# Optimization experiments

Measured on AMD Instinct MI355X. Metric: run time of the kernel, lower is better.

Reference implementation:

```python
import jax, jax.numpy as jnp
import numpy as np

N_NODES = 100000
N_EDGES = 1600000
N_GRAPHS = 256
F_IN = 128
NEURON = 64
AF = 8  # attention_num_feature


def gcn_conv(h_in, W, b, src, dst, n):
    # PyG GCNConv: add self loops, symmetric normalization, XW then aggregate, + bias
    h = h_in @ W  # [N, out]
    loop = jnp.arange(n)
    s = jnp.concatenate([src, loop])
    d = jnp.concatenate([dst, loop])
    deg = jax.ops.segment_sum(jnp.ones(s.shape[0], h.dtype), d, num_segments=n)
    dis = jax.lax.rsqrt(deg)  # deg >= 1 because of self loops
    norm = dis[s] * dis[d]  # [E+N]
    msg = h[s] * norm[:, None]
    out = jax.ops.segment_sum(msg, d, num_segments=n)
    return out + b


def setup_inputs() -> dict:
    key = jax.random.key(0)
    ks = jax.random.split(key, 16)
    x = jax.random.normal(ks[0], (N_NODES, F_IN), dtype=jnp.float32)
    closeness = jax.random.normal(ks[1], (N_NODES, AF), dtype=jnp.float32)
    edge_index = jax.random.randint(ks[2], (2, N_EDGES), 0, N_NODES, dtype=jnp.int64)
    batch = jnp.sort(jax.random.randint(ks[3], (N_NODES,), 0, N_GRAPHS, dtype=jnp.int64))
    def lin(k, fi, fo):
        lim = 1.0 / np.sqrt(fi)
        return jax.random.uniform(k, (fi, fo), jnp.float32, -lim, lim)
    return {
        "x": x, "closeness": closeness,
        "W1": lin(ks[4], F_IN, NEURON), "b1": jnp.zeros((NEURON,), jnp.float32),
        "W2": lin(ks[5], NEURON, NEURON), "b2": jnp.zeros((NEURON,), jnp.float32),
        "W3": lin(ks[6], NEURON, NEURON), "b3": jnp.zeros((NEURON,), jnp.float32),
        "Wc": lin(ks[7], AF, 1), "bc": jnp.zeros((1,), jnp.float32),
        "Wa1": lin(ks[8], NEURON, 16), "ba1": jnp.zeros((16,), jnp.float32),
        "Wa2": lin(ks[9], 16, 1), "ba2": jnp.zeros((1,), jnp.float32),
        "edge_index": edge_index, "batch": batch,
    }


def reference(x, closeness, W1, b1, W2, b2, W3, b3, Wc, bc, Wa1, ba1, Wa2, ba2, edge_index, batch):
    n, G = x.shape[0], N_GRAPHS
    src, dst = edge_index[0], edge_index[1]
    h = jax.nn.relu(gcn_conv(x, W1, b1, src, dst, n))
    h = jax.nn.relu(gcn_conv(h, W2, b2, src, dst, n))
    h = jax.nn.relu(gcn_conv(h, W3, b3, src, dst, n))  # [N, 64]
    # per-graph softmax over closeness logits (vectorized form of the python loop)
    logits = (closeness @ Wc + bc)[:, 0]  # [N]
    m = jax.ops.segment_max(logits, batch, num_segments=G)
    e = jnp.exp(logits - m[batch])
    z = jax.ops.segment_sum(e, batch, num_segments=G)
    p = e / z[batch]  # softmax within each graph
    counts = jax.ops.segment_sum(jnp.ones((n,), h.dtype), batch, num_segments=G)
    counts = jnp.maximum(counts, 1.0)
    attn = p * counts[batch]  # softmax * curr_size
    # self_average: mean over nodes of attn * h  == segment_sum / count
    g = jax.ops.segment_sum(attn[:, None] * h, batch, num_segments=G) / counts[:, None]  # [G, 64]
    a = jax.nn.relu(g @ Wa1 + ba1)
    return a @ Wa2 + ba2  # [G, 1]
```

## Files before the change

kernel.cpp:

```cpp
#include <hip/hip_runtime.h>
#include <hip/hip_fp16.h>
#include <math.h>


#define BKT_SHIFT 7
#define BKT_NODES 128
#define BKT_CAP 4096
#define EPB 8192

typedef _Float16 f16x8 __attribute__((ext_vector_type(8)));
typedef float f32x4 __attribute__((ext_vector_type(4)));

__global__ __launch_bounds__(1024) void block_hist_kernel(
    const int* __restrict__ dst, int* __restrict__ hist, int E, int NBKT, int NBLK) {
  __shared__ int lh[1024];
  const int t = threadIdx.x;
  const int blk = blockIdx.x;
  for (int k = t; k < NBKT; k += 1024) lh[k] = 0;
  __syncthreads();
  const int e0 = blk * EPB;
  const int e1 = min(e0 + EPB, E);
  for (int e = e0 + t; e < e1; e += 1024) atomicAdd(&lh[dst[e] >> BKT_SHIFT], 1);
  __syncthreads();
  for (int k = t; k < NBKT; k += 1024) hist[k * NBLK + blk] = lh[k];
}

__global__ __launch_bounds__(256) void row_scan_kernel(
    const int* __restrict__ hist, int* __restrict__ ebase, int* __restrict__ btot,
    int NBLK) {
  __shared__ int sh[256];
  const int k = blockIdx.x;
  const int t = threadIdx.x;
  int v = (t < NBLK) ? hist[(long)k * NBLK + t] : 0;
  sh[t] = v;
  __syncthreads();
  for (int s = 1; s < 256; s <<= 1) {
    int add = (t >= s) ? sh[t - s] : 0;
    __syncthreads();
    sh[t] += add;
    __syncthreads();
  }
  if (t < NBLK) ebase[(long)k * NBLK + t] = sh[t] - v;
  if (t == 255) btot[k] = sh[255];
}

__global__ __launch_bounds__(1024) void bucket_scan_kernel(
    const int* __restrict__ btot, int* __restrict__ bbase, int E, int NBKT) {
  __shared__ int sh[1024];
  const int t = threadIdx.x;
  int v = (t < NBKT) ? btot[t] : 0;
  sh[t] = v;
  __syncthreads();
  for (int s = 1; s < 1024; s <<= 1) {
    int add = (t >= s) ? sh[t - s] : 0;
    __syncthreads();
    sh[t] += add;
    __syncthreads();
  }
  if (t < NBKT) bbase[t] = sh[t] - v;
  if (t == 0) bbase[NBKT] = E;
}

__global__ __launch_bounds__(1024) void group_kernel(
    const int* __restrict__ src, const int* __restrict__ dst,
    const int* __restrict__ bbase, const int* __restrict__ ebase,
    unsigned int* __restrict__ grouped, int E, int NBKT, int NBLK) {
  __shared__ int lcur[1024];
  const int t = threadIdx.x;
  const int blk = blockIdx.x;
  for (int k = t; k < NBKT; k += 1024)
    lcur[k] = bbase[k] + ebase[(long)k * NBLK + blk];
  __syncthreads();
  const int e0 = blk * EPB;
  const int e1 = min(e0 + EPB, E);
  for (int e = e0 + t; e < e1; e += 1024) {
    int d = dst[e];
    int b = d >> BKT_SHIFT;
    int pos = atomicAdd(&lcur[b], 1);
    grouped[pos] = ((unsigned int)(d & (BKT_NODES - 1)) << 17) | (unsigned int)src[e];
  }
}

__global__ __launch_bounds__(256) void bucket_build_kernel(
    const unsigned int* __restrict__ grouped, const int* __restrict__ bbase,
    int* __restrict__ csr_src, int* __restrict__ ends, float* __restrict__ dis, int N) {
  __shared__ int lcnt[BKT_NODES];
  __shared__ int lsum[BKT_NODES];
  __shared__ int lcur[BKT_NODES];
  __shared__ int stage[BKT_CAP];
  const int b = blockIdx.x;
  const int t = threadIdx.x;
  const int node0 = b << BKT_SHIFT;
  const int nn = min(BKT_NODES, N - node0);
  const int base = bbase[b];
  const int m = bbase[b + 1] - base;

  if (t < BKT_NODES) lcnt[t] = 0;
  __syncthreads();
  for (int i = t; i < m; i += 256) atomicAdd(&lcnt[grouped[base + i] >> 17], 1);
  __syncthreads();
  if (t < BKT_NODES) lsum[t] = lcnt[t];
  __syncthreads();
  for (int s = 1; s < BKT_NODES; s <<= 1) {
    int add = 0;
    if (t < BKT_NODES && t >= s) add = lsum[t - s];
    __syncthreads();
    if (t < BKT_NODES) lsum[t] += add;
    __syncthreads();
  }
  if (t < nn) {
    ends[node0 + t] = base + lsum[t];
    dis[node0 + t] = 1.0f / sqrtf((float)(lcnt[t] + 1));
    lcur[t] = lsum[t] - lcnt[t];
  }
  __syncthreads();
  if (m <= BKT_CAP) {
    for (int i = t; i < m; i += 256) {
      unsigned int v = grouped[base + i];
      int p = atomicAdd(&lcur[v >> 17], 1);
      stage[p] = (int)(v & 0x1FFFFu);
    }
    __syncthreads();
    for (int i = t; i < m; i += 256) csr_src[base + i] = stage[i];
  } else {
    for (int i = t; i < m; i += 256) {
      unsigned int v = grouped[base + i];
      int p = atomicAdd(&lcur[v >> 17], 1);
      csr_src[base + p] = (int)(v & 0x1FFFFu);
    }
  }
}


template <int K, typename Tin>
__global__ __launch_bounds__(256) void gemm_mfma_kernel(
    const Tin* __restrict__ H, const float* __restrict__ W,
    const float* __restrict__ dis, __half* __restrict__ C, int N) {
  __shared__ __align__(16) __half Hs[64 * K];
  __shared__ __align__(16) __half Ws[64 * K];
  const int t = threadIdx.x;
  const int rowBase = blockIdx.x * 64;

  if constexpr (sizeof(Tin) == 4) {
    const int NF4 = 64 * K / 4;
#pragma unroll
    for (int i = 0; i < NF4 / 256; ++i) {
      int f = t + i * 256;
      int row = f / (K / 4);
      int c4 = f % (K / 4);
      int gr = rowBase + row;
      float4 v = make_float4(0.f, 0.f, 0.f, 0.f);
      if (gr < N) v = *reinterpret_cast<const float4*>(H + (long)gr * K + c4 * 4);
      union { uint2 u; __half2 h[2]; } pk;
      pk.h[0] = __floats2half2_rn(v.x, v.y);
      pk.h[1] = __floats2half2_rn(v.z, v.w);
      int byte = (row * K + c4 * 4) * 2;
      byte ^= (row & 7) << 4;
      *reinterpret_cast<uint2*>(reinterpret_cast<char*>(Hs) + byte) = pk.u;
    }
  } else {
    const int NC = 64 * K / 8;
#pragma unroll
    for (int i = 0; i < NC / 256; ++i) {
      int f = t + i * 256;
      int row = f / (K / 8);
      int c8 = f % (K / 8);
      int gr = rowBase + row;
      uint4 v = make_uint4(0u, 0u, 0u, 0u);
      if (gr < N) v = *reinterpret_cast<const uint4*>(H + (long)gr * K + c8 * 8);
      int byte = (row * K + c8 * 8) * 2;
      byte ^= (row & 7) << 4;
      *reinterpret_cast<uint4*>(reinterpret_cast<char*>(Hs) + byte) = v;
    }
  }

  {
    const int NU = (K / 2) * 16;
#pragma unroll
    for (int i = 0; i < NU / 256; ++i) {
      int u = t + i * 256;
      int kp = u >> 4;
      int cq = u & 15;
      const float4 w0 = *reinterpret_cast<const float4*>(W + (long)(2 * kp) * 64 + cq * 4);
      const float4 w1 = *reinterpret_cast<const float4*>(W + (long)(2 * kp + 1) * 64 + cq * 4);
#pragma unroll
      for (int j = 0; j < 4; ++j) {
        int c = cq * 4 + j;
        __half2 p = __floats2half2_rn((&w0.x)[j], (&w1.x)[j]);
        int byte = (c * K + 2 * kp) * 2;
        byte ^= (c & 7) << 4;
        *reinterpret_cast<__half2*>(reinterpret_cast<char*>(Ws) + byte) = p;
      }
    }
  }
  __syncthreads();

  const int w = t >> 6;
  const int l = t & 63;
  const int r = l & 15;
  const int g = l >> 4;
  const int rowL = 16 * w + r;
  f32x4 acc[4] = {{0.f, 0.f, 0.f, 0.f}, {0.f, 0.f, 0.f, 0.f},
                  {0.f, 0.f, 0.f, 0.f}, {0.f, 0.f, 0.f, 0.f}};
#pragma unroll
  for (int s = 0; s < K / 32; ++s) {
    int abyte = (rowL * K + s * 32 + g * 8) * 2;
    abyte ^= (rowL & 7) << 4;
    f16x8 afrag = *reinterpret_cast<const f16x8*>(reinterpret_cast<const char*>(Hs) + abyte);
#pragma unroll
    for (int n = 0; n < 4; ++n) {
      int col = n * 16 + r;
      int bbyte = (col * K + s * 32 + g * 8) * 2;
      bbyte ^= (col & 7) << 4;
      f16x8 bfrag = *reinterpret_cast<const f16x8*>(reinterpret_cast<const char*>(Ws) + bbyte);
      acc[n] = __builtin_amdgcn_mfma_f32_16x16x32_f16(afrag, bfrag, acc[n], 0, 0, 0);
    }
  }

  const int outRow0 = rowBase + 16 * w + 4 * g;
#pragma unroll
  for (int j = 0; j < 4; ++j) {
    int row = outRow0 + j;
    if (row < N) {
      float dv = dis[row];
#pragma unroll
      for (int n = 0; n < 4; ++n) {
        C[(long)row * 64 + n * 16 + r] = __float2half(acc[n][j] * dv);
      }
    }
  }
}


__device__ __forceinline__ float4 h4_to_f4(uint2 u) {
  const __half2 lo = *reinterpret_cast<const __half2*>(&u.x);
  const __half2 hi = *reinterpret_cast<const __half2*>(&u.y);
  const float2 flo = __half22float2(lo);
  const float2 fhi = __half22float2(hi);
  return make_float4(flo.x, flo.y, fhi.x, fhi.y);
}

__global__ __launch_bounds__(256) void aggregate_kernel(
    const __half* __restrict__ Ts, const int* __restrict__ csr_src,
    const int* __restrict__ ends, const float* __restrict__ dis,
    const float* __restrict__ bias, __half* __restrict__ O, int N) {
  int gid = blockIdx.x * 256 + threadIdx.x;
  int d = gid >> 6;
  if (d >= N) return;
  const int lane = threadIdx.x & 63;
  const int q = lane >> 4;
  const int c = lane & 15;
  const int beg = (d == 0) ? 0 : ends[d - 1];
  const int m = ends[d] - beg;
  const uint2* Tv = (const uint2*)Ts;
  const int* sl = csr_src + beg;

  float4 a0 = make_float4(0.f, 0.f, 0.f, 0.f);
  float4 a1 = a0, a2 = a0, a3 = a0;
  if (q == 0) a0 = h4_to_f4(Tv[(long)d * 16 + c]);

  for (int base = 0; base < m; base += 64) {
    const int take = min(m - base, 64);
    int idx = (lane < take) ? sl[base + lane] : 0;
    for (int j = 0; j < take; j += 16) {
      const int l0 = j + q, l1 = j + 4 + q, l2 = j + 8 + q, l3 = j + 12 + q;
      int s0 = __shfl(idx, l0 & 63, 64);
      int s1 = __shfl(idx, l1 & 63, 64);
      int s2 = __shfl(idx, l2 & 63, 64);
      int s3 = __shfl(idx, l3 & 63, 64);
      uint2 r0 = Tv[(long)s0 * 16 + c];
      uint2 r1 = Tv[(long)s1 * 16 + c];
      uint2 r2 = Tv[(long)s2 * 16 + c];
      uint2 r3 = Tv[(long)s3 * 16 + c];
      if (l0 < take) { float4 f = h4_to_f4(r0); a0.x += f.x; a0.y += f.y; a0.z += f.z; a0.w += f.w; }
      if (l1 < take) { float4 f = h4_to_f4(r1); a1.x += f.x; a1.y += f.y; a1.z += f.z; a1.w += f.w; }
      if (l2 < take) { float4 f = h4_to_f4(r2); a2.x += f.x; a2.y += f.y; a2.z += f.z; a2.w += f.w; }
      if (l3 < take) { float4 f = h4_to_f4(r3); a3.x += f.x; a3.y += f.y; a3.z += f.z; a3.w += f.w; }
    }
  }
  a0.x += a1.x; a0.y += a1.y; a0.z += a1.z; a0.w += a1.w;
  a2.x += a3.x; a2.y += a3.y; a2.z += a3.z; a2.w += a3.w;
  a0.x += a2.x; a0.y += a2.y; a0.z += a2.z; a0.w += a2.w;

  a0.x += __shfl_xor(a0.x, 16, 64); a0.y += __shfl_xor(a0.y, 16, 64);
  a0.z += __shfl_xor(a0.z, 16, 64); a0.w += __shfl_xor(a0.w, 16, 64);
  a0.x += __shfl_xor(a0.x, 32, 64); a0.y += __shfl_xor(a0.y, 32, 64);
  a0.z += __shfl_xor(a0.z, 32, 64); a0.w += __shfl_xor(a0.w, 32, 64);

  if (q == 0) {
    float dd = dis[d];
    float4 b4 = ((const float4*)bias)[c];
    union { uint2 u; __half2 h[2]; } pk;
    pk.h[0] = __floats2half2_rn(fmaxf(a0.x * dd + b4.x, 0.f), fmaxf(a0.y * dd + b4.y, 0.f));
    pk.h[1] = __floats2half2_rn(fmaxf(a0.z * dd + b4.z, 0.f), fmaxf(a0.w * dd + b4.w, 0.f));
    ((uint2*)O)[(long)d * 16 + c] = pk.u;
  }
}


__global__ void logits_kernel(const float* __restrict__ clo, const float* __restrict__ Wc,
                              const float* __restrict__ bc, float* __restrict__ lb, int N) {
  int i = blockIdx.x * blockDim.x + threadIdx.x;
  if (i >= N) return;
  float s = bc[0];
#pragma unroll
  for (int k = 0; k < 8; ++k) s += clo[(long)i * 8 + k] * Wc[k];
  lb[i] = s;
}

__global__ __launch_bounds__(256) void pool_kernel(
    const __half* __restrict__ h3, const float* __restrict__ lb,
    const int* __restrict__ batch, const float* __restrict__ Wa1,
    const float* __restrict__ ba1, const float* __restrict__ Wa2,
    const float* __restrict__ ba2, float* __restrict__ out, int N) {
  __shared__ int sLo, sHi;
  __shared__ float red[256];
  __shared__ float Vs[4][64];
  __shared__ float sse[4];
  __shared__ float gv[64];
  __shared__ float am[16];
  const int g = blockIdx.x;
  const int t = threadIdx.x;
  if (t == 0) {
    int lo = 0, hi = N;
    while (lo < hi) { int mid = (lo + hi) >> 1; if (batch[mid] < g) lo = mid + 1; else hi = mid; }
    sLo = lo;
    lo = 0; hi = N;
    while (lo < hi) { int mid = (lo + hi) >> 1; if (batch[mid] < g + 1) lo = mid + 1; else hi = mid; }
    sHi = lo;
  }
  __syncthreads();
  const int lo = sLo, hi = sHi;

  float lm = -1e30f;
  for (int i = lo + t; i < hi; i += 256) lm = fmaxf(lm, lb[i]);
  red[t] = lm;
  __syncthreads();
  for (int s = 128; s > 0; s >>= 1) {
    if (t < s) red[t] = fmaxf(red[t], red[t + s]);
    __syncthreads();
  }
  const float m = red[0];

  const int f = t & 63, sub = t >> 6;
  float vacc = 0.f, seacc = 0.f;
  for (int i = lo + sub; i < hi; i += 4) {
    float e = expf(lb[i] - m);
    seacc += e;
    vacc += e * __half2float(h3[(long)i * 64 + f]);
  }
  Vs[sub][f] = vacc;
  if (f == 0) sse[sub] = seacc;
  __syncthreads();
  if (t < 64) {
    float se = sse[0] + sse[1] + sse[2] + sse[3];
    float v = Vs[0][f] + Vs[1][f] + Vs[2][f] + Vs[3][f];
    gv[f] = (se > 0.f) ? v / se : 0.f;
  }
  __syncthreads();
  if (t < 16) {
    float a = ba1[t];
#pragma unroll
    for (int k2 = 0; k2 < 64; ++k2) a += gv[k2] * Wa1[k2 * 16 + t];
    am[t] = a > 0.f ? a : 0.f;
  }
  __syncthreads();
  if (t == 0) {
    float o = ba2[0];
#pragma unroll
    for (int j = 0; j < 16; ++j) o += am[j] * Wa2[j];
    out[g] = o;
  }
}


extern "C" void kernel_launch(void* const* d_in, const int* in_sizes, int n_in,
                              void* d_out, int out_size, void* d_ws, size_t ws_size,
                              hipStream_t stream) {
  const float* x   = (const float*)d_in[0];
  const float* clo = (const float*)d_in[1];
  const float* W1  = (const float*)d_in[2];
  const float* b1  = (const float*)d_in[3];
  const float* W2  = (const float*)d_in[4];
  const float* b2  = (const float*)d_in[5];
  const float* W3  = (const float*)d_in[6];
  const float* b3  = (const float*)d_in[7];
  const float* Wc  = (const float*)d_in[8];
  const float* bc  = (const float*)d_in[9];
  const float* Wa1 = (const float*)d_in[10];
  const float* ba1 = (const float*)d_in[11];
  const float* Wa2 = (const float*)d_in[12];
  const float* ba2 = (const float*)d_in[13];
  const int* edge  = (const int*)d_in[14];
  const int* batch = (const int*)d_in[15];
  float* out = (float*)d_out;

  const int N = in_sizes[15];
  const int E = in_sizes[14] / 2;
  const int G = out_size;
  const int NBKT = (N + BKT_NODES - 1) >> BKT_SHIFT;
  const int NBLK = (E + EPB - 1) / EPB;

  const int* src = edge;
  const int* dst = edge + E;

  char* p = (char*)d_ws;
  auto alloc = [&](size_t bytes) -> char* {
    char* r = p;
    p += (bytes + 255) & ~(size_t)255;
    return r;
  };
  __half* tsbuf         = (__half*)alloc((size_t)N * 64 * sizeof(__half));
  __half* bufH          = (__half*)alloc((size_t)N * 64 * sizeof(__half));
  int*   csr_src        = (int*)  alloc((size_t)E * sizeof(int));
  unsigned int* grouped = (unsigned int*)alloc((size_t)E * sizeof(unsigned int));
  int*   hist           = (int*)  alloc((size_t)NBKT * NBLK * sizeof(int));
  int*   ebase          = (int*)  alloc((size_t)NBKT * NBLK * sizeof(int));
  int*   btot           = (int*)  alloc((size_t)NBKT * sizeof(int));
  int*   bbase          = (int*)  alloc((size_t)(NBKT + 1) * sizeof(int));
  int*   ends           = (int*)  alloc((size_t)N * sizeof(int));
  float* dis            = (float*)alloc((size_t)N * sizeof(float));
  float* lb             = (float*)alloc((size_t)N * sizeof(float));
  (void)ws_size; (void)n_in;

  block_hist_kernel<<<NBLK, 1024, 0, stream>>>(dst, hist, E, NBKT, NBLK);
  row_scan_kernel<<<NBKT, 256, 0, stream>>>(hist, ebase, btot, NBLK);
  bucket_scan_kernel<<<1, 1024, 0, stream>>>(btot, bbase, E, NBKT);
  group_kernel<<<NBLK, 1024, 0, stream>>>(src, dst, bbase, ebase, grouped, E, NBKT, NBLK);
  bucket_build_kernel<<<NBKT, 256, 0, stream>>>(grouped, bbase, csr_src, ends, dis, N);

  const int gN = (N + 255) / 256;
  const int gGemm = (N + 63) / 64;
  const int gAgg  = (N * 64 + 255) / 256;

  gemm_mfma_kernel<128, float><<<gGemm, 256, 0, stream>>>(x, W1, dis, tsbuf, N);
  aggregate_kernel<<<gAgg, 256, 0, stream>>>(tsbuf, csr_src, ends, dis, b1, bufH, N);
  gemm_mfma_kernel<64, __half><<<gGemm, 256, 0, stream>>>(bufH, W2, dis, tsbuf, N);
  aggregate_kernel<<<gAgg, 256, 0, stream>>>(tsbuf, csr_src, ends, dis, b2, bufH, N);
  gemm_mfma_kernel<64, __half><<<gGemm, 256, 0, stream>>>(bufH, W3, dis, tsbuf, N);
  aggregate_kernel<<<gAgg, 256, 0, stream>>>(tsbuf, csr_src, ends, dis, b3, bufH, N);

  logits_kernel<<<gN, 256, 0, stream>>>(clo, Wc, bc, lb, N);
  pool_kernel<<<G, 256, 0, stream>>>(bufH, lb, batch, Wa1, ba1, Wa2, ba2, out, N);
}
```

Baseline: 352.0 us.

## Aggregate four destination nodes per wavefront with 16 lanes each

The GCN aggregation kernel now assigns one destination node to each 16-lane group, so a 64-lane wavefront handles four nodes instead of one. Each group walks its own neighbour list in chunks of 16, broadcasting source indices with shuffles. This drops the cross-quarter shuffle reduction and cuts the number of wavefronts by four, to improve lane utilisation for the short neighbour lists typical here (about 17 entries). The cost is that all four groups in a wave loop until the longest list finishes, and each group keeps fewer independent loads in flight than the old four-accumulator scheme.

After: 357.9 us. About the same (+1.7%).

```diff
diff --git a/kernel.cpp b/kernel.cpp
--- a/kernel.cpp
+++ b/kernel.cpp
@@ -244,57 +244,44 @@
     const __half* __restrict__ Ts, const int* __restrict__ csr_src,
     const int* __restrict__ ends, const float* __restrict__ dis,
     const float* __restrict__ bias, __half* __restrict__ O, int N) {
-  int gid = blockIdx.x * 256 + threadIdx.x;
-  int d = gid >> 6;
+  const int wid = (blockIdx.x * 256 + threadIdx.x) >> 6;
+  const int l = threadIdx.x & 63;
+  const int g = l >> 4;
+  const int c = l & 15;
+  const int d = wid * 4 + g;
   if (d >= N) return;
-  const int lane = threadIdx.x & 63;
-  const int q = lane >> 4;
-  const int c = lane & 15;
   const int beg = (d == 0) ? 0 : ends[d - 1];
   const int m = ends[d] - beg;
   const uint2* Tv = (const uint2*)Ts;
-  const int* sl = csr_src + beg;
-
-  float4 a0 = make_float4(0.f, 0.f, 0.f, 0.f);
-  float4 a1 = a0, a2 = a0, a3 = a0;
-  if (q == 0) a0 = h4_to_f4(Tv[(long)d * 16 + c]);
-
-  for (int base = 0; base < m; base += 64) {
-    const int take = min(m - base, 64);
-    int idx = (lane < take) ? sl[base + lane] : 0;
-    for (int j = 0; j < take; j += 16) {
-      const int l0 = j + q, l1 = j + 4 + q, l2 = j + 8 + q, l3 = j + 12 + q;
-      int s0 = __shfl(idx, l0 & 63, 64);
-      int s1 = __shfl(idx, l1 & 63, 64);
-      int s2 = __shfl(idx, l2 & 63, 64);
-      int s3 = __shfl(idx, l3 & 63, 64);
-      uint2 r0 = Tv[(long)s0 * 16 + c];
-      uint2 r1 = Tv[(long)s1 * 16 + c];
-      uint2 r2 = Tv[(long)s2 * 16 + c];
-      uint2 r3 = Tv[(long)s3 * 16 + c];
-      if (l0 < take) { float4 f = h4_to_f4(r0); a0.x += f.x; a0.y += f.y; a0.z += f.z; a0.w += f.w; }
-      if (l1 < take) { float4 f = h4_to_f4(r1); a1.x += f.x; a1.y += f.y; a1.z += f.z; a1.w += f.w; }
-      if (l2 < take) { float4 f = h4_to_f4(r2); a2.x += f.x; a2.y += f.y; a2.z += f.z; a2.w += f.w; }
-      if (l3 < take) { float4 f = h4_to_f4(r3); a3.x += f.x; a3.y += f.y; a3.z += f.z; a3.w += f.w; }
-    }
-  }
-  a0.x += a1.x; a0.y += a1.y; a0.z += a1.z; a0.w += a1.w;
-  a2.x += a3.x; a2.y += a3.y; a2.z += a3.z; a2.w += a3.w;
-  a0.x += a2.x; a0.y += a2.y; a0.z += a2.z; a0.w += a2.w;
-
-  a0.x += __shfl_xor(a0.x, 16, 64); a0.y += __shfl_xor(a0.y, 16, 64);
-  a0.z += __shfl_xor(a0.z, 16, 64); a0.w += __shfl_xor(a0.w, 16, 64);
-  a0.x += __shfl_xor(a0.x, 32, 64); a0.y += __shfl_xor(a0.y, 32, 64);
-  a0.z += __shfl_xor(a0.z, 32, 64); a0.w += __shfl_xor(a0.w, 32, 64);
-
-  if (q == 0) {
-    float dd = dis[d];
-    float4 b4 = ((const float4*)bias)[c];
-    union { uint2 u; __half2 h[2]; } pk;
-    pk.h[0] = __floats2half2_rn(fmaxf(a0.x * dd + b4.x, 0.f), fmaxf(a0.y * dd + b4.y, 0.f));
-    pk.h[1] = __floats2half2_rn(fmaxf(a0.z * dd + b4.z, 0.f), fmaxf(a0.w * dd + b4.w, 0.f));
-    ((uint2*)O)[(long)d * 16 + c] = pk.u;
-  }
+
+  float4 a = h4_to_f4(Tv[(long)d * 16 + c]);
+
+  int mmax = m;
+  mmax = max(mmax, __shfl_xor(mmax, 16, 64));
+  mmax = max(mmax, __shfl_xor(mmax, 32, 64));
+
+  const int gbase = l & 48;
+  for (int base = 0; base < mmax; base += 16) {
+    const int take = m - base;
+    int idx = (c < take) ? csr_src[beg + base + c] : 0;
+#pragma unroll 4
+    for (int j = 0; j < 16; ++j) {
+      int s = __shfl(idx, gbase + j, 64);
+      if (j < take) {
+        float4 f = h4_to_f4(Tv[(long)s * 16 + c]);
+        a.x += f.x; a.y += f.y; a.z += f.z; a.w += f.w;
+      }
+    }
+  }
+
+  const float dd = dis[d];
+  const float4 b4 = ((const float4*)bias)[c];
+  union { uint2 uu; __half2 h[2]; } pk;
+  pk.h[0] = __floats2half2_rn(fmaxf(a.x * dd + b4.x, 0.f),
+                              fmaxf(a.y * dd + b4.y, 0.f));
+  pk.h[1] = __floats2half2_rn(fmaxf(a.z * dd + b4.z, 0.f),
+                              fmaxf(a.w * dd + b4.w, 0.f));
+  ((uint2*)O)[(long)d * 16 + c] = pk.uu;
 }
 
 
@@ -431,7 +418,7 @@
 
   const int gN = (N + 255) / 256;
   const int gGemm = (N + 63) / 64;
-  const int gAgg  = (N * 64 + 255) / 256;
+  const int gAgg  = (N + 15) / 16;
 
   gemm_mfma_kernel<128, float><<<gGemm, 256, 0, stream>>>(x, W1, dis, tsbuf, N);
   aggregate_kernel<<<gAgg, 256, 0, stream>>>(tsbuf, csr_src, ends, dis, b1, bufH, N);
```
